# Optimization experiments

Measured on AMD Instinct MI355X. Metric: run time of the kernel, lower is better.

## Reference

```python
import jax, jax.numpy as jnp
import numpy as np

B, T, N, F, H, E = 8, 16, 10000, 64, 64, 1000000
M = B * N  # flattened node count per timestep
NUM_CLASSES = 3


def setup_inputs() -> dict:
    key = jax.random.key(0)
    ks = jax.random.split(key, 10)
    s = 1.0 / np.sqrt(H)
    return {
        "graph_seq": jax.random.normal(ks[0], (B, T, N, F), dtype=jnp.float32),
        "edge_index_seq": jax.random.randint(ks[1], (T, 2, E), 0, M, dtype=jnp.int32),
        "W_gcn": jax.random.normal(ks[2], (F, H), dtype=jnp.float32) / np.sqrt(F),
        "b_gcn": jnp.zeros((H,), dtype=jnp.float32),
        "W_ih": jax.random.uniform(ks[3], (4 * H, H), jnp.float32, -s, s),
        "W_hh": jax.random.uniform(ks[4], (4 * H, H), jnp.float32, -s, s),
        "b_ih": jax.random.uniform(ks[5], (4 * H,), jnp.float32, -s, s),
        "b_hh": jax.random.uniform(ks[6], (4 * H,), jnp.float32, -s, s),
        "W_fc": jax.random.uniform(ks[7], (NUM_CLASSES, H), jnp.float32, -s, s),
        "b_fc": jax.random.uniform(ks[8], (NUM_CLASSES,), jnp.float32, -s, s),
    }


def _forward(graph_seq, edge_index_seq, W_gcn, b_gcn, W_ih, W_hh, b_ih, b_hh, W_fc, b_fc):
    # GCNConv: x' = D^{-1/2}(A+I)D^{-1/2} (x W) + b, applied on flattened (B*N) nodes per timestep.
    xw = jnp.einsum('btnf,fh->btnh', graph_seq, W_gcn)        # [B,T,N,H]
    xw_t = xw.transpose(1, 0, 2, 3).reshape(T, M, H)          # [T, B*N, H], node index = b*N + n

    def gcn_step(_, inp):
        x, ei = inp                                           # x: [M,H], ei: [2,E]
        src, dst = ei[0], ei[1]
        deg = jax.ops.segment_sum(jnp.ones((E,), x.dtype), dst, num_segments=M) + 1.0  # +1 self loop
        dinv = jax.lax.rsqrt(deg)
        coef = dinv[src] * dinv[dst]                          # [E]
        agg = jax.ops.segment_sum(x[src] * coef[:, None], dst, num_segments=M)
        out = agg + x * (dinv * dinv)[:, None] + b_gcn        # self-loop term + bias
        pooled = out.reshape(B, N, H).mean(axis=1)            # mean over nodes -> [B,H]
        return None, pooled

    _, pooled_seq = jax.lax.scan(gcn_step, None, (xw_t, edge_index_seq))  # [T,B,H]

    def lstm_step(carry, x_t):
        h, c = carry
        z = x_t @ W_ih.T + h @ W_hh.T + b_ih + b_hh           # [B,4H], gate order i,f,g,o
        i, f, g, o = jnp.split(z, 4, axis=-1)
        c = jax.nn.sigmoid(f) * c + jax.nn.sigmoid(i) * jnp.tanh(g)
        h = jax.nn.sigmoid(o) * jnp.tanh(c)
        return (h, c), None

    h0 = jnp.zeros((B, H), dtype=graph_seq.dtype)
    (h_last, _), _ = jax.lax.scan(lstm_step, (h0, h0), pooled_seq)
    return h_last @ W_fc.T + b_fc                             # [B,3]


def reference(graph_seq, edge_index_seq, W_gcn, b_gcn, W_ih, W_hh, b_ih, b_hh, W_fc, b_fc):
    return _forward(graph_seq, edge_index_seq, W_gcn, b_gcn, W_ih, W_hh, b_ih, b_hh, W_fc, b_fc)
```

## Files before the change

### kernel.cpp

```cpp
#include <hip/hip_runtime.h>
#include <hip/hip_bf16.h>

#define BB 8
#define TT 16
#define NNODE 10000
#define FF 64
#define HH 64
#define EE 1000000
#define MM 80000
#define NCLS 3

#define NCHUNK 80
#define NPC 1000
#define NSEG_H 16
#define HW 20000
#define NSEG_B 32
#define NW 128
#define EPW 7816
#define WCAP 48
#define FLUSH_THR 24
#define RCAP 176
#define RSZ 177

__global__ __launch_bounds__(256) void k_hist(const int* __restrict__ ei,
                                              unsigned int* __restrict__ part, int t0) {
    __shared__ unsigned int h[HW];
    int seg = blockIdx.x, tloc = blockIdx.y, tg = t0 + tloc;
    for (int i = threadIdx.x; i < HW; i += 256) h[i] = 0u;
    __syncthreads();
    const uint4* dstp = (const uint4*)(ei + (size_t)tg * 2 * EE + EE
                                       + (size_t)seg * (EE / NSEG_H));
    for (int i = threadIdx.x; i < (EE / NSEG_H) / 4; i += 256) {
        uint4 d4 = dstp[i];
        atomicAdd(&h[d4.x >> 2], 1u << ((d4.x & 3u) * 8u));
        atomicAdd(&h[d4.y >> 2], 1u << ((d4.y & 3u) * 8u));
        atomicAdd(&h[d4.z >> 2], 1u << ((d4.z & 3u) * 8u));
        atomicAdd(&h[d4.w >> 2], 1u << ((d4.w & 3u) * 8u));
    }
    __syncthreads();
    unsigned int* outp = part + ((size_t)tloc * NSEG_H + seg) * HW;
    for (int i = threadIdx.x; i < HW; i += 256) outp[i] = h[i];
}

__global__ __launch_bounds__(256) void k_mdeg(const unsigned int* __restrict__ part,
                                              unsigned int* __restrict__ degb) {
    int w = blockIdx.x * 256 + threadIdx.x;
    int tloc = blockIdx.y;
    if (w >= HW) return;
    const unsigned int* p = part + (size_t)tloc * NSEG_H * HW;
    unsigned int s = 0;
#pragma unroll
    for (int k = 0; k < NSEG_H; k++) s += p[(size_t)k * HW + w];
    degb[(size_t)tloc * HW + w] = s;
}

__global__ __launch_bounds__(256) void k_part(const int* __restrict__ ei,
                                              unsigned int* __restrict__ buck, int t0) {
    __shared__ unsigned int stg[4][NCHUNK][WCAP];
    __shared__ unsigned int cur[4][NCHUNK];
    __shared__ unsigned int gct[4][NCHUNK];
    int wave = threadIdx.x >> 6, lane = threadIdx.x & 63;
    int tloc = blockIdx.y, tg = t0 + tloc;
    if (lane < 64) { cur[wave][lane] = 0u; gct[wave][lane] = 0u; }
    if (lane < NCHUNK - 64) { cur[wave][64 + lane] = 0u; gct[wave][64 + lane] = 0u; }

    int wseg = blockIdx.x * 4 + wave;
    int e0 = wseg * EPW;
    int e1 = e0 + EPW; if (e1 > EE) e1 = EE;
    const uint4* src4 = (const uint4*)(ei + (size_t)tg * 2 * EE);
    const uint4* dst4 = (const uint4*)(ei + (size_t)tg * 2 * EE + EE);
    unsigned int* bkt = buck + ((size_t)tloc * NCHUNK * NW + wseg) * RSZ;

    int i40 = e0 >> 2, i41 = e1 >> 2;
    int nIter = (i41 - i40 + 63) >> 6;
    for (int k = 0; k < nIter; k++) {
        int i4 = i40 + k * 64 + lane;
        if (i4 < i41) {
            uint4 s4 = src4[i4];
            uint4 d4 = dst4[i4];
            unsigned int ss[4] = {s4.x, s4.y, s4.z, s4.w};
            unsigned int dd[4] = {d4.x, d4.y, d4.z, d4.w};
#pragma unroll
            for (int j = 0; j < 4; j++) {
                unsigned int ck = (unsigned int)(((unsigned long long)ss[j] * 4294968ull) >> 32);
                unsigned int so = ss[j] - ck * NPC;
                unsigned int p = atomicAdd(&cur[wave][ck], 1u);
                if (p < WCAP) stg[wave][ck][p] = (so << 17) | dd[j];
            }
        }
#pragma unroll
        for (int half = 0; half < 2; half++) {
            int nh = half ? (NCHUNK - 64) : 64;
            unsigned int cnt = (lane < nh) ? cur[wave][half * 64 + lane] : 0u;
            unsigned long long mask = __ballot(cnt >= FLUSH_THR);
            while (mask) {
                int ck = half * 64 + (__ffsll((unsigned long long)mask) - 1);
                mask &= mask - 1;
                unsigned int n = cur[wave][ck];
                if (n > WCAP) n = WCAP;
                unsigned int gp = gct[wave][ck];
                unsigned int nw = (gp + n <= RCAP) ? n : ((gp < RCAP) ? (RCAP - gp) : 0u);
                unsigned int* rg = bkt + (size_t)ck * NW * RSZ;
                if (lane < nw) rg[1 + gp + lane] = stg[wave][ck][lane];
                if (lane == 0) { gct[wave][ck] = gp + nw; cur[wave][ck] = 0u; }
            }
        }
    }
    for (int ck = 0; ck < NCHUNK; ck++) {
        unsigned int n = cur[wave][ck];
        if (n > WCAP) n = WCAP;
        if (n > 0u) {
            unsigned int gp = gct[wave][ck];
            unsigned int nw = (gp + n <= RCAP) ? n : ((gp < RCAP) ? (RCAP - gp) : 0u);
            unsigned int* rg = bkt + (size_t)ck * NW * RSZ;
            if (lane < nw) rg[1 + gp + lane] = stg[wave][ck][lane];
            if (lane == 0) gct[wave][ck] = gp + nw;
        }
    }
    for (int ck = lane; ck < NCHUNK; ck += 64)
        bkt[(size_t)ck * NW * RSZ] = gct[wave][ck];
}

__global__ __launch_bounds__(512) void k_scat(const float* __restrict__ g,
                                              const unsigned int* __restrict__ degb,
                                              const unsigned int* __restrict__ buck,
                                              float* __restrict__ yp, int t0) {
    __shared__ float a[NPC * BB];
    __shared__ float lut[256];
    int c = blockIdx.x, tloc = blockIdx.y, tg = t0 + tloc;
    int wave = threadIdx.x >> 6, lane = threadIdx.x & 63;

    for (int i = threadIdx.x; i < NPC * BB; i += 512) a[i] = 0.0f;
    if (threadIdx.x < 256) lut[threadIdx.x] = rsqrtf((float)threadIdx.x + 1.0f);
    __syncthreads();

    const unsigned char* degc = (const unsigned char*)(degb + (size_t)tloc * HW);
    const unsigned int* bkc = buck + ((size_t)tloc * NCHUNK + c) * NW * RSZ;

    for (int r = wave; r < NW; r += 8) {
        const unsigned int* rg = bkc + (size_t)r * RSZ;
        unsigned int cnt = rg[0];
        if (cnt > RCAP) cnt = RCAP;
        for (unsigned int i = lane; i < cnt; i += 64) {
            unsigned int rec = rg[1 + i];
            unsigned int d = rec & 0x1FFFFu;
            unsigned int so = rec >> 17;
            unsigned int b = (unsigned int)(((unsigned long long)d * 429497ull) >> 32);
            atomicAdd(&a[so * BB + b], lut[degc[d]]);
        }
    }
    __syncthreads();

    int b_c = c / 10, coff = c - b_c * 10;
    int jbase = c * NPC;
    for (int j = threadIdx.x; j < NPC; j += 512) {
        float dvj = lut[degc[jbase + j]];
        float* aj = &a[j * BB];
#pragma unroll
        for (int b = 0; b < BB; b++)
            aj[b] = dvj * (aj[b] + (b == b_c ? dvj : 0.0f));
    }
    __syncthreads();

    int sub = lane >> 4;
    int f0 = (lane & 15) << 2;
    const float* gbase = g + ((size_t)(b_c * TT + tg) * NNODE + (size_t)coff * NPC) * FF;

    float acc[BB][4];
#pragma unroll
    for (int b = 0; b < BB; b++)
#pragma unroll
        for (int q = 0; q < 4; q++) acc[b][q] = 0.0f;

    const int NG = NPC / 4;
    for (int gi = wave; gi < NG; gi += 16) {
        int j0 = gi * 4 + sub;
        int gi1 = gi + 8;
        int j1 = gi1 * 4 + sub;
        bool h1 = (gi1 < NG);
        const float4 g40 = *(const float4*)(gbase + (size_t)j0 * FF + f0);
        float4 g41 = h1 ? *(const float4*)(gbase + (size_t)j1 * FF + f0)
                        : make_float4(0.f, 0.f, 0.f, 0.f);
        {
            const float4 a0 = *(const float4*)(&a[j0 * BB]);
            const float4 a1 = *(const float4*)(&a[j0 * BB + 4]);
            float av[BB] = {a0.x, a0.y, a0.z, a0.w, a1.x, a1.y, a1.z, a1.w};
#pragma unroll
            for (int b = 0; b < BB; b++) {
                acc[b][0] = fmaf(g40.x, av[b], acc[b][0]);
                acc[b][1] = fmaf(g40.y, av[b], acc[b][1]);
                acc[b][2] = fmaf(g40.z, av[b], acc[b][2]);
                acc[b][3] = fmaf(g40.w, av[b], acc[b][3]);
            }
        }
        if (h1) {
            const float4 a0 = *(const float4*)(&a[j1 * BB]);
            const float4 a1 = *(const float4*)(&a[j1 * BB + 4]);
            float av[BB] = {a0.x, a0.y, a0.z, a0.w, a1.x, a1.y, a1.z, a1.w};
#pragma unroll
            for (int b = 0; b < BB; b++) {
                acc[b][0] = fmaf(g41.x, av[b], acc[b][0]);
                acc[b][1] = fmaf(g41.y, av[b], acc[b][1]);
                acc[b][2] = fmaf(g41.z, av[b], acc[b][2]);
                acc[b][3] = fmaf(g41.w, av[b], acc[b][3]);
            }
        }
    }

    __syncthreads();
#pragma unroll
    for (int b = 0; b < BB; b++)
#pragma unroll
        for (int q = 0; q < 4; q++) {
            float v = acc[b][q];
            v += __shfl_xor(v, 16);
            v += __shfl_xor(v, 32);
            acc[b][q] = v;
        }
    if (sub == 0) {
#pragma unroll
        for (int b = 0; b < BB; b++)
#pragma unroll
            for (int q = 0; q < 4; q++)
                a[wave * (BB * FF) + b * FF + f0 + q] = acc[b][q];
    }
    __syncthreads();
    {
        int idx = threadIdx.x;
        float s = 0.0f;
#pragma unroll
        for (int w = 0; w < 8; w++) s += a[w * (BB * FF) + idx];
        yp[((size_t)tg * NCHUNK + c) * (BB * FF) + idx] = s;
    }
}

__global__ __launch_bounds__(512) void k_fold(const float* __restrict__ yp,
                                              float* __restrict__ y2) {
    int t = blockIdx.x;
    int idx = threadIdx.x;
    const float* p = yp + (size_t)t * NCHUNK * BB * FF + idx;
    float s = 0.0f;
#pragma unroll 8
    for (int u = 0; u < NCHUNK; u++) s += p[(size_t)u * BB * FF];
    y2[(size_t)t * BB * FF + idx] = s;
}

__global__ __launch_bounds__(256) void k_lstm(const float* __restrict__ y2,
                                              const float* __restrict__ Wg,
                                              const float* __restrict__ bg,
                                              const float* __restrict__ Wih,
                                              const float* __restrict__ Whh,
                                              const float* __restrict__ bih,
                                              const float* __restrict__ bhh,
                                              const float* __restrict__ Wfc,
                                              const float* __restrict__ bfc,
                                              float* __restrict__ out) {
    int b = blockIdx.x;
    int r = threadIdx.x;

    __shared__ float xs[TT][HH];
    __shared__ float hs[HH], cs[HH], zs[4 * HH];

    for (int idx = r; idx < TT * HH; idx += 256) {
        int t = idx >> 6, h = idx & 63;
        const float* yt = y2 + ((size_t)t * BB + b) * FF;
        float s = 0.0f;
#pragma unroll
        for (int f = 0; f < FF; f++) s = fmaf(yt[f], Wg[f * HH + h], s);
        xs[t][h] = s * (1.0f / NNODE) + bg[h];
    }

    float wih[HH], whh[HH];
#pragma unroll
    for (int k = 0; k < HH; k++) {
        wih[k] = Wih[r * HH + k];
        whh[k] = Whh[r * HH + k];
    }
    float bias = bih[r] + bhh[r];

    if (r < HH) { hs[r] = 0.0f; cs[r] = 0.0f; }
    __syncthreads();

    for (int t = 0; t < TT; t++) {
        float acc = bias;
#pragma unroll
        for (int k = 0; k < HH; k++)
            acc = fmaf(wih[k], xs[t][k], fmaf(whh[k], hs[k], acc));
        zs[r] = acc;
        __syncthreads();
        if (r < HH) {
            float iv = zs[r], fv = zs[HH + r], gv = zs[2 * HH + r], ov = zs[3 * HH + r];
            float si = 1.0f / (1.0f + expf(-iv));
            float sf = 1.0f / (1.0f + expf(-fv));
            float so = 1.0f / (1.0f + expf(-ov));
            float cc = sf * cs[r] + si * tanhf(gv);
            cs[r] = cc;
            hs[r] = so * tanhf(cc);
        }
        __syncthreads();
    }

    if (r < NCLS) {
        float s = bfc[r];
#pragma unroll
        for (int k = 0; k < HH; k++) s = fmaf(hs[k], Wfc[r * HH + k], s);
        out[b * NCLS + r] = s;
    }
}

extern "C" void kernel_launch(void* const* d_in, const int* in_sizes, int n_in,
                              void* d_out, int out_size, void* d_ws, size_t ws_size,
                              hipStream_t stream) {
    const float* g   = (const float*)d_in[0];
    const int*   ei  = (const int*)d_in[1];
    const float* Wg  = (const float*)d_in[2];
    const float* bg  = (const float*)d_in[3];
    const float* Wih = (const float*)d_in[4];
    const float* Whh = (const float*)d_in[5];
    const float* bih = (const float*)d_in[6];
    const float* bhh = (const float*)d_in[7];
    const float* Wfc = (const float*)d_in[8];
    const float* bfc = (const float*)d_in[9];
    float* out = (float*)d_out;

    char* ws = (char*)d_ws;
    float* yp = (float*)ws;
    const size_t ypBytes = (size_t)TT * NCHUNK * BB * FF * sizeof(float);
    float* y2 = (float*)(ws + ypBytes);
    const size_t y2Bytes = (size_t)TT * BB * FF * sizeof(float);
    const size_t headBytes = ypBytes + y2Bytes;

    const size_t sz_part = (size_t)NSEG_H * HW * 4;
    const size_t sz_degb = (size_t)HW * 4;
    const size_t sz_buck = (size_t)NCHUNK * NW * RSZ * 4;
    const size_t per_t = sz_part + sz_degb + sz_buck;

    size_t avail = (ws_size > headBytes) ? ws_size - headBytes : 0;
    int Tg = (int)(avail / per_t);
    if (Tg > TT) Tg = TT;
    if (Tg < 1) Tg = 1;

    size_t ofs = headBytes;
    unsigned int* part = (unsigned int*)(ws + ofs); ofs += (size_t)Tg * sz_part;
    unsigned int* degb = (unsigned int*)(ws + ofs); ofs += (size_t)Tg * sz_degb;
    unsigned int* buck = (unsigned int*)(ws + ofs);

    for (int t0 = 0; t0 < TT; t0 += Tg) {
        int tc = (TT - t0 < Tg) ? (TT - t0) : Tg;

        dim3 gh(NSEG_H, tc);
        k_hist<<<gh, 256, 0, stream>>>(ei, part, t0);

        dim3 gm((HW + 255) / 256, tc);
        k_mdeg<<<gm, 256, 0, stream>>>(part, degb);

        dim3 gp(NSEG_B, tc);
        k_part<<<gp, 256, 0, stream>>>(ei, buck, t0);

        dim3 gs(NCHUNK, tc);
        k_scat<<<gs, 512, 0, stream>>>(g, degb, buck, yp, t0);
    }

    k_fold<<<TT, 512, 0, stream>>>(yp, y2);
    k_lstm<<<BB, 256, 0, stream>>>(y2, Wg, bg, Wih, Whh, bih, bhh, Wfc, bfc, out);
}
```

Baseline: 331.9 us.

## Split bucket counts into header array and vectorize bucket record reads

Each bucket's count moves out of its slot into a separate header array, and bucket capacity shrinks to a 16-byte-aligned size. The scatter kernel stages the counts in shared memory and reads each row's records with one uint4 load per lane instead of a strided scalar loop. This cuts workspace size and the number of load instructions. In exchange, the smaller capacity raises the chance that records are silently truncated if a bucket overflows.

```diff
diff --git a/kernel.cpp b/kernel.cpp
--- a/kernel.cpp
+++ b/kernel.cpp
@@ -19,8 +19,7 @@
 #define EPW 7816
 #define WCAP 48
 #define FLUSH_THR 24
-#define RCAP 176
-#define RSZ 177
+#define RCAP 152
 
 __global__ __launch_bounds__(256) void k_hist(const int* __restrict__ ei,
                                               unsigned int* __restrict__ part, int t0) {
@@ -55,7 +54,8 @@
 }
 
 __global__ __launch_bounds__(256) void k_part(const int* __restrict__ ei,
-                                              unsigned int* __restrict__ buck, int t0) {
+                                              unsigned int* __restrict__ buck,
+                                              unsigned int* __restrict__ hdr, int t0) {
     __shared__ unsigned int stg[4][NCHUNK][WCAP];
     __shared__ unsigned int cur[4][NCHUNK];
     __shared__ unsigned int gct[4][NCHUNK];
@@ -69,7 +69,7 @@
     int e1 = e0 + EPW; if (e1 > EE) e1 = EE;
     const uint4* src4 = (const uint4*)(ei + (size_t)tg * 2 * EE);
     const uint4* dst4 = (const uint4*)(ei + (size_t)tg * 2 * EE + EE);
-    unsigned int* bkt = buck + ((size_t)tloc * NCHUNK * NW + wseg) * RSZ;
+    unsigned int* bkt = buck + ((size_t)tloc * NCHUNK * NW + wseg) * RCAP;
 
     int i40 = e0 >> 2, i41 = e1 >> 2;
     int nIter = (i41 - i40 + 63) >> 6;
@@ -100,8 +100,8 @@
                 if (n > WCAP) n = WCAP;
                 unsigned int gp = gct[wave][ck];
                 unsigned int nw = (gp + n <= RCAP) ? n : ((gp < RCAP) ? (RCAP - gp) : 0u);
-                unsigned int* rg = bkt + (size_t)ck * NW * RSZ;
-                if (lane < nw) rg[1 + gp + lane] = stg[wave][ck][lane];
+                unsigned int* rg = bkt + (size_t)ck * NW * RCAP;
+                if (lane < nw) rg[gp + lane] = stg[wave][ck][lane];
                 if (lane == 0) { gct[wave][ck] = gp + nw; cur[wave][ck] = 0u; }
             }
         }
@@ -112,41 +112,53 @@
         if (n > 0u) {
             unsigned int gp = gct[wave][ck];
             unsigned int nw = (gp + n <= RCAP) ? n : ((gp < RCAP) ? (RCAP - gp) : 0u);
-            unsigned int* rg = bkt + (size_t)ck * NW * RSZ;
-            if (lane < nw) rg[1 + gp + lane] = stg[wave][ck][lane];
+            unsigned int* rg = bkt + (size_t)ck * NW * RCAP;
+            if (lane < nw) rg[gp + lane] = stg[wave][ck][lane];
             if (lane == 0) gct[wave][ck] = gp + nw;
         }
     }
     for (int ck = lane; ck < NCHUNK; ck += 64)
-        bkt[(size_t)ck * NW * RSZ] = gct[wave][ck];
+        hdr[((size_t)tloc * NCHUNK + ck) * NW + wseg] = gct[wave][ck];
 }
 
 __global__ __launch_bounds__(512) void k_scat(const float* __restrict__ g,
                                               const unsigned int* __restrict__ degb,
                                               const unsigned int* __restrict__ buck,
+                                              const unsigned int* __restrict__ hdr,
                                               float* __restrict__ yp, int t0) {
     __shared__ float a[NPC * BB];
     __shared__ float lut[256];
+    __shared__ unsigned int hcnt[NW];
     int c = blockIdx.x, tloc = blockIdx.y, tg = t0 + tloc;
     int wave = threadIdx.x >> 6, lane = threadIdx.x & 63;
 
     for (int i = threadIdx.x; i < NPC * BB; i += 512) a[i] = 0.0f;
     if (threadIdx.x < 256) lut[threadIdx.x] = rsqrtf((float)threadIdx.x + 1.0f);
+    if (threadIdx.x < NW)
+        hcnt[threadIdx.x] = hdr[((size_t)tloc * NCHUNK + c) * NW + threadIdx.x];
     __syncthreads();
 
     const unsigned char* degc = (const unsigned char*)(degb + (size_t)tloc * HW);
-    const unsigned int* bkc = buck + ((size_t)tloc * NCHUNK + c) * NW * RSZ;
+    const unsigned int* bkc = buck + ((size_t)tloc * NCHUNK + c) * NW * RCAP;
 
     for (int r = wave; r < NW; r += 8) {
-        const unsigned int* rg = bkc + (size_t)r * RSZ;
-        unsigned int cnt = rg[0];
+        unsigned int cnt = hcnt[r];
         if (cnt > RCAP) cnt = RCAP;
-        for (unsigned int i = lane; i < cnt; i += 64) {
-            unsigned int rec = rg[1 + i];
-            unsigned int d = rec & 0x1FFFFu;
-            unsigned int so = rec >> 17;
-            unsigned int b = (unsigned int)(((unsigned long long)d * 429497ull) >> 32);
-            atomicAdd(&a[so * BB + b], lut[degc[d]]);
+        const uint4* rg4 = (const uint4*)(bkc + (size_t)r * RCAP);
+        unsigned int i0 = lane << 2;
+        if (i0 < cnt) {
+            uint4 rr = rg4[lane];
+            unsigned int recs[4] = {rr.x, rr.y, rr.z, rr.w};
+#pragma unroll
+            for (int k = 0; k < 4; k++) {
+                if (i0 + (unsigned)k < cnt) {
+                    unsigned int rec = recs[k];
+                    unsigned int d = rec & 0x1FFFFu;
+                    unsigned int so = rec >> 17;
+                    unsigned int b = (unsigned int)(((unsigned long long)d * 429497ull) >> 32);
+                    atomicAdd(&a[so * BB + b], lut[degc[d]]);
+                }
+            }
         }
     }
     __syncthreads();
@@ -332,8 +344,9 @@
 
     const size_t sz_part = (size_t)NSEG_H * HW * 4;
     const size_t sz_degb = (size_t)HW * 4;
-    const size_t sz_buck = (size_t)NCHUNK * NW * RSZ * 4;
-    const size_t per_t = sz_part + sz_degb + sz_buck;
+    const size_t sz_buck = (size_t)NCHUNK * NW * RCAP * 4;
+    const size_t sz_hdr  = (size_t)NCHUNK * NW * 4;
+    const size_t per_t = sz_part + sz_degb + sz_buck + sz_hdr;
 
     size_t avail = (ws_size > headBytes) ? ws_size - headBytes : 0;
     int Tg = (int)(avail / per_t);
@@ -343,6 +356,7 @@
     size_t ofs = headBytes;
     unsigned int* part = (unsigned int*)(ws + ofs); ofs += (size_t)Tg * sz_part;
     unsigned int* degb = (unsigned int*)(ws + ofs); ofs += (size_t)Tg * sz_degb;
+    unsigned int* hdr  = (unsigned int*)(ws + ofs); ofs += (size_t)Tg * sz_hdr;
     unsigned int* buck = (unsigned int*)(ws + ofs);
 
     for (int t0 = 0; t0 < TT; t0 += Tg) {
@@ -355,10 +369,10 @@
         k_mdeg<<<gm, 256, 0, stream>>>(part, degb);
 
         dim3 gp(NSEG_B, tc);
-        k_part<<<gp, 256, 0, stream>>>(ei, buck, t0);
+        k_part<<<gp, 256, 0, stream>>>(ei, buck, hdr, t0);
 
         dim3 gs(NCHUNK, tc);
-        k_scat<<<gs, 512, 0, stream>>>(g, degb, buck, yp, t0);
+        k_scat<<<gs, 512, 0, stream>>>(g, degb, buck, hdr, yp, t0);
     }
 
     k_fold<<<TT, 512, 0, stream>>>(yp, y2);
```

Result: faster. 322.8 us (-2.8%).

## Pad edge buckets with sentinel records and unroll the feature gather loop

Applied to the files above, without the earlier changes.

Edge buckets drop their count header and become fixed-size (RCAP shrinks from 176 to 152). Unused slots are filled with sentinel records that point to extra dummy rows in the shared accumulator, so k_scat can stream the whole bucket region with uniform uint4 loads instead of per-row, count-bounded scalar loops. The feature-gather loop in k_scat is also unrolled to issue four global float4 loads before the FMAs. The trade-off is extra atomic work on sentinel records, contention on the 16 dummy addresses, and a higher chance that a bucket overflows and drops edges with the smaller capacity.

```diff
diff --git a/kernel.cpp b/kernel.cpp
--- a/kernel.cpp
+++ b/kernel.cpp
@@ -19,8 +19,8 @@
 #define EPW 7816
 #define WCAP 48
 #define FLUSH_THR 24
-#define RCAP 176
-#define RSZ 177
+#define RCAP 152
+#define AROWS 1024
 
 __global__ __launch_bounds__(256) void k_hist(const int* __restrict__ ei,
                                               unsigned int* __restrict__ part, int t0) {
@@ -69,7 +69,7 @@
     int e1 = e0 + EPW; if (e1 > EE) e1 = EE;
     const uint4* src4 = (const uint4*)(ei + (size_t)tg * 2 * EE);
     const uint4* dst4 = (const uint4*)(ei + (size_t)tg * 2 * EE + EE);
-    unsigned int* bkt = buck + ((size_t)tloc * NCHUNK * NW + wseg) * RSZ;
+    unsigned int* bkt = buck + ((size_t)tloc * NCHUNK * NW + wseg) * RCAP;
 
     int i40 = e0 >> 2, i41 = e1 >> 2;
     int nIter = (i41 - i40 + 63) >> 6;
@@ -100,49 +100,52 @@
                 if (n > WCAP) n = WCAP;
                 unsigned int gp = gct[wave][ck];
                 unsigned int nw = (gp + n <= RCAP) ? n : ((gp < RCAP) ? (RCAP - gp) : 0u);
-                unsigned int* rg = bkt + (size_t)ck * NW * RSZ;
-                if (lane < nw) rg[1 + gp + lane] = stg[wave][ck][lane];
+                unsigned int* rg = bkt + (size_t)ck * NW * RCAP;
+                if (lane < nw) rg[gp + lane] = stg[wave][ck][lane];
                 if (lane == 0) { gct[wave][ck] = gp + nw; cur[wave][ck] = 0u; }
             }
         }
     }
+    unsigned int sv = (1008u + (lane & 15u)) << 17;
     for (int ck = 0; ck < NCHUNK; ck++) {
         unsigned int n = cur[wave][ck];
         if (n > WCAP) n = WCAP;
+        unsigned int gp = gct[wave][ck];
+        unsigned int* rg = bkt + (size_t)ck * NW * RCAP;
+        unsigned int nw = 0;
         if (n > 0u) {
-            unsigned int gp = gct[wave][ck];
-            unsigned int nw = (gp + n <= RCAP) ? n : ((gp < RCAP) ? (RCAP - gp) : 0u);
-            unsigned int* rg = bkt + (size_t)ck * NW * RSZ;
-            if (lane < nw) rg[1 + gp + lane] = stg[wave][ck][lane];
-            if (lane == 0) gct[wave][ck] = gp + nw;
-        }
-    }
-    for (int ck = lane; ck < NCHUNK; ck += 64)
-        bkt[(size_t)ck * NW * RSZ] = gct[wave][ck];
+            nw = (gp + n <= RCAP) ? n : ((gp < RCAP) ? (RCAP - gp) : 0u);
+            if (lane < nw) rg[gp + lane] = stg[wave][ck][lane];
+        }
+        for (unsigned int j = gp + nw + lane; j < RCAP; j += 64)
+            rg[j] = sv;
+    }
 }
 
 __global__ __launch_bounds__(512) void k_scat(const float* __restrict__ g,
                                               const unsigned int* __restrict__ degb,
                                               const unsigned int* __restrict__ buck,
                                               float* __restrict__ yp, int t0) {
-    __shared__ float a[NPC * BB];
+    __shared__ float a[AROWS * BB];
     __shared__ float lut[256];
     int c = blockIdx.x, tloc = blockIdx.y, tg = t0 + tloc;
     int wave = threadIdx.x >> 6, lane = threadIdx.x & 63;
 
-    for (int i = threadIdx.x; i < NPC * BB; i += 512) a[i] = 0.0f;
+    for (int i = threadIdx.x; i < AROWS * BB; i += 512) a[i] = 0.0f;
     if (threadIdx.x < 256) lut[threadIdx.x] = rsqrtf((float)threadIdx.x + 1.0f);
     __syncthreads();
 
     const unsigned char* degc = (const unsigned char*)(degb + (size_t)tloc * HW);
-    const unsigned int* bkc = buck + ((size_t)tloc * NCHUNK + c) * NW * RSZ;
-
-    for (int r = wave; r < NW; r += 8) {
-        const unsigned int* rg = bkc + (size_t)r * RSZ;
-        unsigned int cnt = rg[0];
-        if (cnt > RCAP) cnt = RCAP;
-        for (unsigned int i = lane; i < cnt; i += 64) {
-            unsigned int rec = rg[1 + i];
+    const unsigned int* bkc = buck + ((size_t)tloc * NCHUNK + c) * NW * RCAP;
+
+    const uint4* bk4 = (const uint4*)bkc;
+    const int NB4 = NW * RCAP / 4;
+    for (int i = threadIdx.x; i < NB4; i += 512) {
+        uint4 r = bk4[i];
+        unsigned int recs[4] = {r.x, r.y, r.z, r.w};
+#pragma unroll
+        for (int k = 0; k < 4; k++) {
+            unsigned int rec = recs[k];
             unsigned int d = rec & 0x1FFFFu;
             unsigned int so = rec >> 17;
             unsigned int b = (unsigned int)(((unsigned long long)d * 429497ull) >> 32);
@@ -172,40 +175,42 @@
 #pragma unroll
         for (int q = 0; q < 4; q++) acc[b][q] = 0.0f;
 
+#define PROC(J, G)                                                          \
+    {                                                                       \
+        const float4 a0 = *(const float4*)(&a[(J) * BB]);                   \
+        const float4 a1 = *(const float4*)(&a[(J) * BB + 4]);               \
+        float av[BB] = {a0.x, a0.y, a0.z, a0.w, a1.x, a1.y, a1.z, a1.w};    \
+        _Pragma("unroll")                                                   \
+        for (int b = 0; b < BB; b++) {                                      \
+            acc[b][0] = fmaf((G).x, av[b], acc[b][0]);                      \
+            acc[b][1] = fmaf((G).y, av[b], acc[b][1]);                      \
+            acc[b][2] = fmaf((G).z, av[b], acc[b][2]);                      \
+            acc[b][3] = fmaf((G).w, av[b], acc[b][3]);                      \
+        }                                                                   \
+    }
+
     const int NG = NPC / 4;
-    for (int gi = wave; gi < NG; gi += 16) {
+    int gi = wave;
+    for (; gi + 24 < NG; gi += 32) {
         int j0 = gi * 4 + sub;
-        int gi1 = gi + 8;
-        int j1 = gi1 * 4 + sub;
-        bool h1 = (gi1 < NG);
-        const float4 g40 = *(const float4*)(gbase + (size_t)j0 * FF + f0);
-        float4 g41 = h1 ? *(const float4*)(gbase + (size_t)j1 * FF + f0)
-                        : make_float4(0.f, 0.f, 0.f, 0.f);
-        {
-            const float4 a0 = *(const float4*)(&a[j0 * BB]);
-            const float4 a1 = *(const float4*)(&a[j0 * BB + 4]);
-            float av[BB] = {a0.x, a0.y, a0.z, a0.w, a1.x, a1.y, a1.z, a1.w};
-#pragma unroll
-            for (int b = 0; b < BB; b++) {
-                acc[b][0] = fmaf(g40.x, av[b], acc[b][0]);
-                acc[b][1] = fmaf(g40.y, av[b], acc[b][1]);
-                acc[b][2] = fmaf(g40.z, av[b], acc[b][2]);
-                acc[b][3] = fmaf(g40.w, av[b], acc[b][3]);
-            }
-        }
-        if (h1) {
-            const float4 a0 = *(const float4*)(&a[j1 * BB]);
-            const float4 a1 = *(const float4*)(&a[j1 * BB + 4]);
-            float av[BB] = {a0.x, a0.y, a0.z, a0.w, a1.x, a1.y, a1.z, a1.w};
-#pragma unroll
-            for (int b = 0; b < BB; b++) {
-                acc[b][0] = fmaf(g41.x, av[b], acc[b][0]);
-                acc[b][1] = fmaf(g41.y, av[b], acc[b][1]);
-                acc[b][2] = fmaf(g41.z, av[b], acc[b][2]);
-                acc[b][3] = fmaf(g41.w, av[b], acc[b][3]);
-            }
-        }
-    }
+        int j1 = (gi + 8) * 4 + sub;
+        int j2 = (gi + 16) * 4 + sub;
+        int j3 = (gi + 24) * 4 + sub;
+        const float4 G0 = *(const float4*)(gbase + (size_t)j0 * FF + f0);
+        const float4 G1 = *(const float4*)(gbase + (size_t)j1 * FF + f0);
+        const float4 G2 = *(const float4*)(gbase + (size_t)j2 * FF + f0);
+        const float4 G3 = *(const float4*)(gbase + (size_t)j3 * FF + f0);
+        PROC(j0, G0);
+        PROC(j1, G1);
+        PROC(j2, G2);
+        PROC(j3, G3);
+    }
+    for (; gi < NG; gi += 8) {
+        int j = gi * 4 + sub;
+        const float4 G = *(const float4*)(gbase + (size_t)j * FF + f0);
+        PROC(j, G);
+    }
+#undef PROC
 
     __syncthreads();
 #pragma unroll
@@ -332,7 +337,7 @@
 
     const size_t sz_part = (size_t)NSEG_H * HW * 4;
     const size_t sz_degb = (size_t)HW * 4;
-    const size_t sz_buck = (size_t)NCHUNK * NW * RSZ * 4;
+    const size_t sz_buck = (size_t)NCHUNK * NW * RCAP * 4;
     const size_t per_t = sz_part + sz_degb + sz_buck;
 
     size_t avail = (ws_size > headBytes) ? ws_size - headBytes : 0;
```

After: 353.1 us. 6.4% more time.
